# Performance work log

Measured on AMD Instinct MI355X. Metric: run time of the kernel, lower is better.

The kernel has to match this reference:

```python
import math
import jax, jax.numpy as jnp
import numpy as np

B, CIN, COUT, K, Z, H, W = 8, 512, 512, 3, 512, 64, 64


def setup_inputs() -> dict:
    key = jax.random.key(0)
    k1, k2, k3, k4 = jax.random.split(key, 4)
    inp = {
        "input": jax.random.normal(k1, (B, CIN, H, W), dtype=jnp.float32),
        "style": jax.random.normal(k2, (B, Z), dtype=jnp.float32),
        # base conv weight: [1, out, in, k, k]
        "weight": jax.random.normal(k3, (1, COUT, CIN, K, K), dtype=jnp.float32),
        # EqualLinear modulation params (lr_mul=1, bias_init=1)
        "mod_w": jax.random.normal(k4, (CIN, Z), dtype=jnp.float32),
        "mod_b": jnp.ones((CIN,), dtype=jnp.float32),
    }
    return inp


def reference(input, style, weight, mod_w, mod_b):
    # EqualLinear: scale = 1/sqrt(z_dim), lr_mul = 1, no activation
    z_dim = mod_w.shape[1]
    mod_scale = 1.0 / math.sqrt(z_dim)
    s = style @ (mod_w * mod_scale).T + mod_b  # [B, in]

    # modulated per-sample weights: scale * base_weight * style
    in_ch, k = weight.shape[2], weight.shape[-1]
    conv_scale = 1.0 / math.sqrt(in_ch * k * k)
    w = conv_scale * weight * s[:, None, :, None, None]  # [B, out, in, k, k]

    pad = k // 2

    def conv_one(x, wb):  # x: [in, H, W], wb: [out, in, k, k]
        return jax.lax.conv_general_dilated(
            x[None], wb, window_strides=(1, 1),
            padding=[(pad, pad), (pad, pad)],
            dimension_numbers=("NCHW", "OIHW", "NCHW"),
        )[0]

    out = jax.vmap(conv_one)(input, w)  # [B, out, H, W]
    return out
```

## Files before the change

### kernel.cpp

```cpp
#include <hip/hip_runtime.h>
#include <hip/hip_bf16.h>

#define BB   8
#define CIN  512
#define COUT 512
#define ZD   512
#define HH   64
#define WW   64

#define MOD_SCALE  0.04419417382415922f
#define CONV_SCALE 0.014731391274719742f

typedef __bf16 bf16x8 __attribute__((ext_vector_type(8)));
typedef float  f32x4  __attribute__((ext_vector_type(4)));

static __device__ __forceinline__ unsigned short f32_to_bf16_rne(float f) {
    unsigned int u = __float_as_uint(f);
    u = (u + 0x7FFFu + ((u >> 16) & 1u)) >> 16;
    return (unsigned short)u;
}

__global__ void k_style(const float* __restrict__ style, const float* __restrict__ mod_w,
                        const float* __restrict__ mod_b, float* __restrict__ sconv) {
    int wid  = blockIdx.x * 4 + (threadIdx.x >> 6);
    int lane = threadIdx.x & 63;
    int b = wid >> 9;
    int i = wid & 511;
    const float4* st = (const float4*)(style + (size_t)b * ZD);
    const float4* mw = (const float4*)(mod_w + (size_t)i * ZD);
    float4 a0 = st[lane],      b0 = mw[lane];
    float4 a1 = st[lane + 64], b1 = mw[lane + 64];
    float sum = a0.x*b0.x + a0.y*b0.y + a0.z*b0.z + a0.w*b0.w
              + a1.x*b1.x + a1.y*b1.y + a1.z*b1.z + a1.w*b1.w;
    #pragma unroll
    for (int off = 32; off > 0; off >>= 1) sum += __shfl_down(sum, off);
    if (lane == 0) sconv[wid] = (sum * MOD_SCALE + mod_b[i]) * CONV_SCALE;
}

__global__ void k_zero_border(unsigned short* __restrict__ xs2p) {
    int b = blockIdx.y;
    int p = blockIdx.x * 4 + (threadIdx.x >> 6);
    int lane = threadIdx.x & 63;
    int h, w;
    if (p < 66)       { h = 0;       w = p; }
    else if (p < 132) { h = 65;      w = p - 66; }
    else if (p < 196) { h = p - 131; w = 0; }
    else              { h = p - 195; w = 65; }
    int4 z = {0, 0, 0, 0};
    *(int4*)&xs2p[((size_t)(b * 66 + h) * 66 + w) * 512 + lane * 8] = z;
}

__global__ void k_scale_input(const float* __restrict__ input, const float* __restrict__ sconv,
                              unsigned short* __restrict__ xs2p) {
    int i0 = blockIdx.x * 32;
    int h  = blockIdx.y;
    int b  = blockIdx.z;
    __shared__ unsigned short lds[64][40];
    #pragma unroll
    for (int r = 0; r < 8; ++r) {
        int ii = r * 4 + (threadIdx.x >> 6);
        int w  = threadIdx.x & 63;
        float v = input[(((size_t)b * CIN + i0 + ii) * HH + h) * WW + w];
        float s = sconv[b * CIN + i0 + ii];
        lds[w][ii] = f32_to_bf16_rne(v * s);
    }
    __syncthreads();
    int w = threadIdx.x >> 2, q = threadIdx.x & 3;
    int4 val = *(const int4*)&lds[w][q * 8];
    *(int4*)&xs2p[((size_t)(b * 66 + h + 1) * 66 + (w + 1)) * 512 + i0 + q * 8] = val;
}

__global__ void k_weight(const float* __restrict__ weight, unsigned short* __restrict__ w3) {
    int t = blockIdx.x * 256 + threadIdx.x;
    int o = t >> 9, i = t & 511;
    int c = i >> 5, g = (i >> 3) & 3, il = i & 7;
    int h = o >> 8, ol = o & 255;
    const float* src = weight + ((size_t)o * CIN + i) * 9;
    #pragma unroll
    for (int p = 0; p < 9; ++p) {
        size_t gran = ((size_t)(c * 9 + p) * 2 + h) * 1024 + g * 256 + ol;
        w3[gran * 8 + il] = f32_to_bf16_rne(src[p]);
    }
}

#define GLD(srcp, ldsbyte)                                                        \
    __builtin_amdgcn_global_load_lds(                                             \
        (const __attribute__((address_space(1))) unsigned int*)(srcp),            \
        (__attribute__((address_space(3))) unsigned int*)(smb + (ldsbyte)),       \
        16, 0, 0)

#define TAP(T, VMA, DOX, DOW) {                                                   \
    const int ko_ = ((T) / 3) * (66 * 16) + ((T) % 3) * 16;                       \
    const int wwr_ = (wrd + 49152) & 65535;                                       \
    if (DOW) GLD(pW, wwr_ + wdst);                                                \
    if ((DOX) && (T) == 0) GLD(sxn +  0, xwr + 0 * 8192 + wdst);                  \
    if ((DOX) && (T) == 1) GLD(sxn + 32, xwr + 2 * 8192 + wdst);                  \
    {   const char* wb = smb + wrd + aoff;                                        \
        const char* xb = smb + xrd + boff + ko_;                                  \
        _Pragma("unroll") for (int mt = 0; mt < 4; ++mt)                          \
            afr[mt] = *(const bf16x8*)(wb + mt * 256);                            \
        _Pragma("unroll") for (int nt = 0; nt < 4; ++nt)                          \
            bfr[nt] = *(const bf16x8*)(xb + nt * 256);                            \
    }                                                                             \
    __builtin_amdgcn_s_barrier();                                                 \
    __builtin_amdgcn_s_setprio(1);                                                \
    _Pragma("unroll") for (int mt = 0; mt < 4; ++mt)                              \
        _Pragma("unroll") for (int nt = 0; nt < 4; ++nt)                          \
            acc[mt][nt] = __builtin_amdgcn_mfma_f32_16x16x32_bf16(                \
                afr[mt], bfr[nt], acc[mt][nt], 0, 0, 0);                          \
    __builtin_amdgcn_s_setprio(0);                                                \
    __builtin_amdgcn_s_barrier();                                                 \
    if (DOW) GLD(pW + 8192, wwr_ + 8192 + wdst);                                  \
    if ((DOX) && (T) == 0) GLD(sxn + 16, xwr + 1 * 8192 + wdst);                  \
    if ((DOX) && (T) == 1) GLD(sxn + 48, xwr + 3 * 8192 + wdst);                  \
    {   const char* wb = smb + wrd + aoff + 1024;                                 \
        _Pragma("unroll") for (int mt = 0; mt < 4; ++mt)                          \
            afr[mt] = *(const bf16x8*)(wb + mt * 256);                            \
    }                                                                             \
    __builtin_amdgcn_s_barrier();                                                 \
    __builtin_amdgcn_s_setprio(1);                                                \
    _Pragma("unroll") for (int mt = 0; mt < 4; ++mt)                              \
        _Pragma("unroll") for (int nt = 0; nt < 4; ++nt)                          \
            acc[4 + mt][nt] = __builtin_amdgcn_mfma_f32_16x16x32_bf16(            \
                afr[mt], bfr[nt], acc[4 + mt][nt], 0, 0, 0);                      \
    __builtin_amdgcn_s_setprio(0);                                                \
    asm volatile("s_waitcnt vmcnt(" #VMA ")" ::: "memory");                       \
    __builtin_amdgcn_s_barrier();                                                 \
    wrd = (wrd + 16384) & 65535;                                                  \
    if (DOW) pW += 32768;                                                         \
}

__global__ __launch_bounds__(512, 2)
void k_conv(const unsigned short* __restrict__ xs2p, const unsigned short* __restrict__ w3,
            float* __restrict__ out) {
    __shared__ unsigned short smem[65536];
    char* smb = (char*)smem;

    const int tid  = threadIdx.x;
    const int wid  = tid >> 6, lane = tid & 63;
    const int wm   = wid >> 2, wr   = wid & 3;
    const int lm   = lane & 15, hi  = lane >> 4;
    const int half = blockIdx.x;
    const int oc0  = half * 256;
    const int y0   = blockIdx.y * 4;
    const int b    = blockIdx.z;

    const int p_lin = wid * 64 + lane;
    const int xrow  = p_lin / 66;
    const int xcol  = p_lin - xrow * 66;
    const char* srcX = (const char*)xs2p;
    if (p_lin < 396)
        srcX += ((size_t)(b * 66 + y0 + xrow) * 66 + xcol) * 1024;

    const char* pW0 = (const char*)w3 + (size_t)half * 16384 + p_lin * 16;
    const int wdst = p_lin * 16;

    GLD(srcX +  0, 65536 + 0 * 8192 + wdst);
    GLD(srcX + 16, 65536 + 1 * 8192 + wdst);
    GLD(srcX + 32, 65536 + 2 * 8192 + wdst);
    GLD(srcX + 48, 65536 + 3 * 8192 + wdst);
    GLD(pW0,          0     + wdst);
    GLD(pW0 +  8192,  8192  + wdst);
    GLD(pW0 + 32768,  16384 + wdst);
    GLD(pW0 + 40960,  24576 + wdst);
    GLD(pW0 + 65536,  32768 + wdst);
    GLD(pW0 + 73728,  40960 + wdst);
    const char* pW = pW0 + 3 * 32768;
    asm volatile("s_waitcnt vmcnt(4)" ::: "memory");
    __builtin_amdgcn_s_barrier();

    f32x4 acc[8][4];
    #pragma unroll
    for (int mt = 0; mt < 8; ++mt)
        #pragma unroll
        for (int nt = 0; nt < 4; ++nt)
            acc[mt][nt] = (f32x4){0.f, 0.f, 0.f, 0.f};

    const int aoff = hi * 4096 + (wm * 128 + lm) * 16;
    const int boff = hi * 8192 + (wr * 66 + lm) * 16;

    bf16x8 afr[4], bfr[4];
    int wrd = 0;
    int xrd = 65536;
    const char* sxn = srcX + 64;

    for (int c = 0; c < 15; ++c) {
        const int xwr = xrd ^ 32768;
        TAP(0, 6, 1, 1) TAP(1, 8, 1, 1) TAP(2, 7, 0, 1) TAP(3, 5, 0, 1)
        TAP(4, 4, 0, 1) TAP(5, 4, 0, 1) TAP(6, 4, 0, 1) TAP(7, 4, 0, 1)
        TAP(8, 4, 0, 1)
        sxn += 64; xrd ^= 32768;
    }
    {
        const int xwr = 0; (void)xwr;
        TAP(0, 4, 0, 1) TAP(1, 4, 0, 1) TAP(2, 4, 0, 1) TAP(3, 4, 0, 1)
        TAP(4, 4, 0, 1) TAP(5, 4, 0, 1) TAP(6, 2, 0, 0) TAP(7, 0, 0, 0)
        TAP(8, 0, 0, 0)
    }

    const int ybase = (y0 + wr) * 64;
    #pragma unroll
    for (int mt = 0; mt < 8; ++mt)
        #pragma unroll
        for (int nt = 0; nt < 4; ++nt)
            #pragma unroll
            for (int r = 0; r < 4; ++r) {
                int oc = oc0 + wm * 128 + mt * 16 + hi * 4 + r;
                out[((size_t)(b * COUT + oc) << 12) + ybase + nt * 16 + lm] = acc[mt][nt][r];
            }
}

extern "C" void kernel_launch(void* const* d_in, const int* in_sizes, int n_in,
                              void* d_out, int out_size, void* d_ws, size_t ws_size,
                              hipStream_t stream) {
    const float* input  = (const float*)d_in[0];
    const float* style  = (const float*)d_in[1];
    const float* weight = (const float*)d_in[2];
    const float* mod_w  = (const float*)d_in[3];
    const float* mod_b  = (const float*)d_in[4];
    float* out = (float*)d_out;

    const size_t xs2p_bytes = (size_t)BB * 66 * 66 * 512 * 2;
    const size_t w3_bytes   = (size_t)144 * 2 * 1024 * 8 * 2;
    const size_t need = 16384 + xs2p_bytes + w3_bytes;
    if (ws_size < need) return;

    float*          sconv = (float*)d_ws;
    unsigned short* xs2p  = (unsigned short*)((char*)d_ws + 16384);
    unsigned short* w3    = (unsigned short*)((char*)d_ws + 16384 + xs2p_bytes);

    hipLaunchKernelGGL(k_style,       dim3(1024),      dim3(256), 0, stream, style, mod_w, mod_b, sconv);
    hipLaunchKernelGGL(k_weight,      dim3(1024),      dim3(256), 0, stream, weight, w3);
    hipLaunchKernelGGL(k_zero_border, dim3(65, 8),     dim3(256), 0, stream, xs2p);
    hipLaunchKernelGGL(k_scale_input, dim3(16, 64, 8), dim3(256), 0, stream, input, sconv, xs2p);
    hipLaunchKernelGGL(k_conv,        dim3(2, 16, 8),  dim3(512), 0, stream, xs2p, w3, out);
}
```

Before: 157.3 us.

## Switch conv GEMM to 32x32x16 MFMA with double-buffered register fragments

```diff
diff --git a/kernel.cpp b/kernel.cpp
--- a/kernel.cpp
+++ b/kernel.cpp
@@ -13,6 +13,7 @@
 
 typedef __bf16 bf16x8 __attribute__((ext_vector_type(8)));
 typedef float  f32x4  __attribute__((ext_vector_type(4)));
+typedef float  f32x16 __attribute__((ext_vector_type(16)));
 
 static __device__ __forceinline__ unsigned short f32_to_bf16_rne(float f) {
     unsigned int u = __float_as_uint(f);
@@ -89,45 +90,50 @@
         (__attribute__((address_space(3))) unsigned int*)(smb + (ldsbyte)),       \
         16, 0, 0)
 
-#define TAP(T, VMA, DOX, DOW) {                                                   \
-    const int ko_ = ((T) / 3) * (66 * 16) + ((T) % 3) * 16;                       \
-    const int wwr_ = (wrd + 49152) & 65535;                                       \
-    if (DOW) GLD(pW, wwr_ + wdst);                                                \
-    if ((DOX) && (T) == 0) GLD(sxn +  0, xwr + 0 * 8192 + wdst);                  \
-    if ((DOX) && (T) == 1) GLD(sxn + 32, xwr + 2 * 8192 + wdst);                  \
-    {   const char* wb = smb + wrd + aoff;                                        \
-        const char* xb = smb + xrd + boff + ko_;                                  \
-        _Pragma("unroll") for (int mt = 0; mt < 4; ++mt)                          \
-            afr[mt] = *(const bf16x8*)(wb + mt * 256);                            \
-        _Pragma("unroll") for (int nt = 0; nt < 4; ++nt)                          \
-            bfr[nt] = *(const bf16x8*)(xb + nt * 256);                            \
+#define MFMA8(Af, Bf)                                                             \
+    _Pragma("unroll") for (int mt = 0; mt < 4; ++mt)                              \
+        _Pragma("unroll") for (int nt = 0; nt < 2; ++nt)                          \
+            acc[mt][nt] = __builtin_amdgcn_mfma_f32_32x32x16_bf16(                \
+                Af[mt], Bf[nt], acc[mt][nt], 0, 0, 0);
+
+#define TAP(t, Nmid, DOX, DOW, LASTTS) {                                          \
+    const int kh0 = (t) / 3, kw0 = (t) % 3;                                       \
+    const int tn  = ((t) + 1) % 9;                                                \
+    const int kh1 = tn / 3, kw1 = tn % 3;                                         \
+    const int wnx = (wrd + 16384) & 65535;                                        \
+    const int wwr = (wrd + 49152) & 65535;                                        \
+    const int xrdn = ((t) == 8) ? (xrd ^ 32768) : xrd;                            \
+                                  \
+    if ((DOX) && (t) == 0) GLD(sxn +  0, xwr + 0 * 8192 + wdst);                  \
+    if ((DOX) && (t) == 1) GLD(sxn + 32, xwr + 2 * 8192 + wdst);                  \
+    if (DOW) GLD(pW, wwr + wdst);                                                 \
+    {   const char* wb = smb + wrd + 8192 + aoff;                                 \
+        const char* xb = smb + xrd + 16384 + boff + kh0 * 1056 + kw0 * 16;        \
+        aB[0] = *(const bf16x8*)(wb);        aB[1] = *(const bf16x8*)(wb + 512);  \
+        aB[2] = *(const bf16x8*)(wb + 1024); aB[3] = *(const bf16x8*)(wb + 1536); \
+        bB[0] = *(const bf16x8*)(xb);        bB[1] = *(const bf16x8*)(xb + 512);  \
     }                                                                             \
+    __builtin_amdgcn_s_setprio(1);                                                \
+    MFMA8(aA, bA)                                                                 \
+    __builtin_amdgcn_s_setprio(0);                                                \
+    asm volatile("s_waitcnt vmcnt(" #Nmid ")" ::: "memory");                      \
     __builtin_amdgcn_s_barrier();                                                 \
+                                  \
+    if ((DOX) && (t) == 0) GLD(sxn + 16, xwr + 1 * 8192 + wdst);                  \
+    if ((DOX) && (t) == 1) GLD(sxn + 48, xwr + 3 * 8192 + wdst);                  \
+    if (DOW) { GLD(pW + 8192, wwr + 8192 + wdst); pW += 32768; }                  \
+    if (!(LASTTS)) {                                                              \
+        const char* wb = smb + wnx + aoff;                                        \
+        const char* xb = smb + xrdn + boff + kh1 * 1056 + kw1 * 16;               \
+        aA[0] = *(const bf16x8*)(wb);        aA[1] = *(const bf16x8*)(wb + 512);  \
+        aA[2] = *(const bf16x8*)(wb + 1024); aA[3] = *(const bf16x8*)(wb + 1536); \
+        bA[0] = *(const bf16x8*)(xb);        bA[1] = *(const bf16x8*)(xb + 512);  \
+    }                                                                             \
     __builtin_amdgcn_s_setprio(1);                                                \
-    _Pragma("unroll") for (int mt = 0; mt < 4; ++mt)                              \
-        _Pragma("unroll") for (int nt = 0; nt < 4; ++nt)                          \
-            acc[mt][nt] = __builtin_amdgcn_mfma_f32_16x16x32_bf16(                \
-                afr[mt], bfr[nt], acc[mt][nt], 0, 0, 0);                          \
+    MFMA8(aB, bB)                                                                 \
     __builtin_amdgcn_s_setprio(0);                                                \
     __builtin_amdgcn_s_barrier();                                                 \
-    if (DOW) GLD(pW + 8192, wwr_ + 8192 + wdst);                                  \
-    if ((DOX) && (T) == 0) GLD(sxn + 16, xwr + 1 * 8192 + wdst);                  \
-    if ((DOX) && (T) == 1) GLD(sxn + 48, xwr + 3 * 8192 + wdst);                  \
-    {   const char* wb = smb + wrd + aoff + 1024;                                 \
-        _Pragma("unroll") for (int mt = 0; mt < 4; ++mt)                          \
-            afr[mt] = *(const bf16x8*)(wb + mt * 256);                            \
-    }                                                                             \
-    __builtin_amdgcn_s_barrier();                                                 \
-    __builtin_amdgcn_s_setprio(1);                                                \
-    _Pragma("unroll") for (int mt = 0; mt < 4; ++mt)                              \
-        _Pragma("unroll") for (int nt = 0; nt < 4; ++nt)                          \
-            acc[4 + mt][nt] = __builtin_amdgcn_mfma_f32_16x16x32_bf16(            \
-                afr[mt], bfr[nt], acc[4 + mt][nt], 0, 0, 0);                      \
-    __builtin_amdgcn_s_setprio(0);                                                \
-    asm volatile("s_waitcnt vmcnt(" #VMA ")" ::: "memory");                       \
-    __builtin_amdgcn_s_barrier();                                                 \
-    wrd = (wrd + 16384) & 65535;                                                  \
-    if (DOW) pW += 32768;                                                         \
+    wrd = wnx;                                                                    \
 }
 
 __global__ __launch_bounds__(512, 2)
@@ -139,7 +145,7 @@
     const int tid  = threadIdx.x;
     const int wid  = tid >> 6, lane = tid & 63;
     const int wm   = wid >> 2, wr   = wid & 3;
-    const int lm   = lane & 15, hi  = lane >> 4;
+    const int l31  = lane & 31, l5  = lane >> 5;
     const int half = blockIdx.x;
     const int oc0  = half * 256;
     const int y0   = blockIdx.y * 4;
@@ -169,44 +175,53 @@
     asm volatile("s_waitcnt vmcnt(4)" ::: "memory");
     __builtin_amdgcn_s_barrier();
 
-    f32x4 acc[8][4];
-    #pragma unroll
-    for (int mt = 0; mt < 8; ++mt)
+    f32x16 acc[4][2];
+    #pragma unroll
+    for (int mt = 0; mt < 4; ++mt)
         #pragma unroll
-        for (int nt = 0; nt < 4; ++nt)
-            acc[mt][nt] = (f32x4){0.f, 0.f, 0.f, 0.f};
-
-    const int aoff = hi * 4096 + (wm * 128 + lm) * 16;
-    const int boff = hi * 8192 + (wr * 66 + lm) * 16;
-
-    bf16x8 afr[4], bfr[4];
+        for (int nt = 0; nt < 2; ++nt)
+            acc[mt][nt] = (f32x16)(0.f);
+
+    const int aoff = l5 * 4096 + (wm * 128 + l31) * 16;
+    const int boff = l5 * 8192 + (wr * 66 + l31) * 16;
+
+    bf16x8 aA[4], bA[2], aB[4], bB[2];
     int wrd = 0;
     int xrd = 65536;
     const char* sxn = srcX + 64;
 
+    {
+        const char* wb = smb + aoff;
+        const char* xb = smb + 65536 + boff;
+        aA[0] = *(const bf16x8*)(wb);        aA[1] = *(const bf16x8*)(wb + 512);
+        aA[2] = *(const bf16x8*)(wb + 1024); aA[3] = *(const bf16x8*)(wb + 1536);
+        bA[0] = *(const bf16x8*)(xb);        bA[1] = *(const bf16x8*)(xb + 512);
+    }
+
     for (int c = 0; c < 15; ++c) {
         const int xwr = xrd ^ 32768;
-        TAP(0, 6, 1, 1) TAP(1, 8, 1, 1) TAP(2, 7, 0, 1) TAP(3, 5, 0, 1)
-        TAP(4, 4, 0, 1) TAP(5, 4, 0, 1) TAP(6, 4, 0, 1) TAP(7, 4, 0, 1)
-        TAP(8, 4, 0, 1)
+        TAP(0, 4, 1, 1, 0) TAP(1, 6, 1, 1, 0) TAP(2, 5, 0, 1, 0)
+        TAP(3, 3, 0, 1, 0) TAP(4, 3, 0, 1, 0) TAP(5, 3, 0, 1, 0)
+        TAP(6, 3, 0, 1, 0) TAP(7, 3, 0, 1, 0) TAP(8, 3, 0, 1, 0)
         sxn += 64; xrd ^= 32768;
     }
     {
         const int xwr = 0; (void)xwr;
-        TAP(0, 4, 0, 1) TAP(1, 4, 0, 1) TAP(2, 4, 0, 1) TAP(3, 4, 0, 1)
-        TAP(4, 4, 0, 1) TAP(5, 4, 0, 1) TAP(6, 2, 0, 0) TAP(7, 0, 0, 0)
-        TAP(8, 0, 0, 0)
+        TAP(0, 3, 0, 1, 0) TAP(1, 3, 0, 1, 0) TAP(2, 3, 0, 1, 0)
+        TAP(3, 3, 0, 1, 0) TAP(4, 3, 0, 1, 0) TAP(5, 3, 0, 1, 0)
+        TAP(6, 2, 0, 0, 0) TAP(7, 0, 0, 0, 0) TAP(8, 0, 0, 0, 1)
     }
 
     const int ybase = (y0 + wr) * 64;
     #pragma unroll
-    for (int mt = 0; mt < 8; ++mt)
+    for (int mt = 0; mt < 4; ++mt)
         #pragma unroll
-        for (int nt = 0; nt < 4; ++nt)
+        for (int nt = 0; nt < 2; ++nt)
             #pragma unroll
-            for (int r = 0; r < 4; ++r) {
-                int oc = oc0 + wm * 128 + mt * 16 + hi * 4 + r;
-                out[((size_t)(b * COUT + oc) << 12) + ybase + nt * 16 + lm] = acc[mt][nt][r];
+            for (int r = 0; r < 16; ++r) {
+                int row = (r & 3) + 8 * (r >> 2) + 4 * l5;
+                int oc  = oc0 + wm * 128 + mt * 32 + row;
+                out[((size_t)(b * COUT + oc) << 12) + ybase + nt * 32 + l31] = acc[mt][nt][r];
             }
 }
 
```

Result: slower. 165.9 us (+5.4%).
